# Optimization experiments

Measured on AMD Instinct MI355X. Metric: run time of the kernel, lower is better.

Reference implementation:

```python
import jax, jax.numpy as jnp
import numpy as np

N_NODES = 100000


def gcn_conv(x, edge_index, W, b, n_nodes):
    # PyG GCNConv: h = x @ W; add self-loops; symmetric normalization; aggregate to dst; + bias
    h = x @ W  # [N, out]
    loop = jnp.arange(n_nodes, dtype=edge_index.dtype)
    src = jnp.concatenate([edge_index[0], loop])
    dst = jnp.concatenate([edge_index[1], loop])
    ones = jnp.ones(src.shape[0], dtype=h.dtype)
    deg = jax.ops.segment_sum(ones, dst, num_segments=n_nodes)  # in-degree incl. self-loop
    dinv = jnp.where(deg > 0, jax.lax.rsqrt(deg), 0.0)
    norm = dinv[src] * dinv[dst]  # [E+N]
    msgs = h[src] * norm[:, None]  # gather + scale
    out = jax.ops.segment_sum(msgs, dst, num_segments=n_nodes)  # scatter-add
    return out + b


def setup_inputs() -> dict:
    key = jax.random.key(0)
    k1, k2, k3, k4 = jax.random.split(key, 4)
    x = jax.random.normal(k1, (N_NODES, 256), dtype=jnp.float32)
    edge_index = jax.random.randint(k2, (2, 3200000), 0, N_NODES, dtype=jnp.int64)
    W1 = jax.random.normal(k3, (256, 64), dtype=jnp.float32) * (1.0 / np.sqrt(256))
    b1 = jnp.zeros((64,), dtype=jnp.float32)
    W2 = jax.random.normal(k4, (64, 40), dtype=jnp.float32) * (1.0 / np.sqrt(64))
    b2 = jnp.zeros((40,), dtype=jnp.float32)
    return {"x": x, "edge_index": edge_index, "W1": W1, "b1": b1, "W2": W2, "b2": b2}


def reference(x, edge_index, W1, b1, W2, b2):
    n = x.shape[0]
    h = gcn_conv(x, edge_index, W1, b1, n)
    h = jax.nn.relu(h)
    h = gcn_conv(h, edge_index, W2, b2, n)
    return jax.nn.log_softmax(h, axis=1)
```

## Files before the change

kernel.cpp:

```cpp
#include <hip/hip_runtime.h>
#include <hip/hip_bf16.h>
#include <math.h>

static constexpr int NN    = 100000;
static constexpr int BSH   = 9;
static constexpr int NBUCK = (NN + 511) >> 9;
static constexpr int EPB   = 8192;
static constexpr int CAP   = 24576;

typedef __attribute__((ext_vector_type(8))) short short8;
typedef __attribute__((ext_vector_type(4))) float f32x4;
typedef __attribute__((ext_vector_type(2))) float f32x2;

#if defined(__has_builtin)
#  if __has_builtin(__builtin_amdgcn_cvt_pk_f32_fp8) && __has_builtin(__builtin_amdgcn_cvt_pk_fp8_f32)
#    define USE_HW_FP8 1
#  endif
#endif
#ifndef USE_HW_FP8
#  define USE_HW_FP8 0
#endif

__device__ __forceinline__ short f2bf(float f) {
    __hip_bfloat16 h = __float2bfloat16(f);
    return __builtin_bit_cast(short, h);
}

__device__ __forceinline__ float fp8_dec_sw(unsigned b) {
    unsigned u = ((b & 0x80u) << 24) | ((b & 0x7Fu) << 20);
    return __builtin_bit_cast(float, u) * 0x1p120f;
}
__device__ __forceinline__ unsigned fp8_enc_sw(float f) {
    unsigned u = __builtin_bit_cast(unsigned, f * 0x1p-120f);
    unsigned s = (u >> 24) & 0x80u;
    unsigned mag = u & 0x7FFFFFFFu;
    unsigned t = mag + 0x7FFFFu + ((mag >> 20) & 1u);
    unsigned r = t >> 20;
    if (r > 0x7Eu) r = 0x7Eu;
    return s | r;
}

template<bool HI>
__device__ __forceinline__ f32x2 dec2w(unsigned u) {
#if USE_HW_FP8
    return __builtin_amdgcn_cvt_pk_f32_fp8(u, HI);
#else
    unsigned w = HI ? (u >> 16) : u;
    f32x2 r;
    r.x = fp8_dec_sw(w & 0xFFu);
    r.y = fp8_dec_sw((w >> 8) & 0xFFu);
    return r;
#endif
}
__device__ __forceinline__ unsigned enc2(float a, float b) {
#if USE_HW_FP8
    return (unsigned)__builtin_amdgcn_cvt_pk_fp8_f32(a, b, 0, false);
#else
    return fp8_enc_sw(a) | (fp8_enc_sw(b) << 8);
#endif
}

__device__ __forceinline__ void acc8(f32x2* a, uint2 u) {
    a[0] += dec2w<false>(u.x);
    a[1] += dec2w<true>(u.x);
    a[2] += dec2w<false>(u.y);
    a[3] += dec2w<true>(u.y);
}
__device__ __forceinline__ void acc8s(f32x2* a, uint2 u, float ds) {
    f32x2 w = {ds, ds};
    a[0] = dec2w<false>(u.x) * w + a[0];
    a[1] = dec2w<true>(u.x)  * w + a[1];
    a[2] = dec2w<false>(u.y) * w + a[2];
    a[3] = dec2w<true>(u.y)  * w + a[3];
}

__device__ __forceinline__ long long ldidx(const void* __restrict__ p, long long i, int is64) {
    if (is64) return ((const long long* __restrict__)p)[i];
    return (long long)((const int* __restrict__)p)[i];
}

template<int K, int NCOLS, int KT, int NT>
__device__ __forceinline__ void packB_dev(const float* __restrict__ W,
                                          short* __restrict__ P, int t) {
    if (t >= KT * NT * 64) return;
    int kt = t / (NT * 64);
    int nt = (t / 64) % NT;
    int l  = t & 63;
    int g  = l >> 4;
#pragma unroll
    for (int e = 0; e < 8; ++e) {
        int k   = kt * 32 + g * 8 + e;
        int col = nt * 16 + (l & 15);
        float v = (col < NCOLS) ? W[k * NCOLS + col] : 0.0f;
        P[t * 8 + e] = f2bf(v);
    }
}

__global__ void __launch_bounds__(256)
k_init(const unsigned int* __restrict__ e32, int* __restrict__ flag,
       int* __restrict__ gcur,
       const float* __restrict__ W1, short* __restrict__ pB1,
       const float* __restrict__ W2, short* __restrict__ pB2) {
    int blk = blockIdx.x, tid = threadIdx.x;
    if (blk == 0) {
        if (tid < NBUCK) gcur[tid] = 0;
        __shared__ int any_nz;
        if (tid == 0) any_nz = 0;
        __syncthreads();
        unsigned int nz = 0;
        for (int w = 1 + 2 * tid; w < 4096; w += 512)
            nz |= e32[w];
        if (nz) atomicOr(&any_nz, 1);
        __syncthreads();
        if (tid == 0) *flag = (any_nz == 0) ? 1 : 0;
    } else if (blk <= 8) {
        packB_dev<256, 64, 8, 4>(W1, pB1, (blk - 1) * 256 + tid);
    } else {
        packB_dev<64, 40, 2, 3>(W2, pB2, (blk - 9) * 256 + tid);
    }
}

__global__ void __launch_bounds__(1024)
k_build_gemm1(const void* __restrict__ eidx, const int* __restrict__ flag, long long E,
              int nsblk, int ngblk, int* __restrict__ gcur, unsigned* __restrict__ ebuf,
              const float* __restrict__ X, const short* __restrict__ pB1,
              unsigned char* __restrict__ H, int n) {
    int bid = (int)blockIdx.x;
    int mn = nsblk < ngblk ? nsblk : ngblk;
    int role, idx;
    if (bid < 2 * mn) { role = bid & 1; idx = bid >> 1; }
    else {
        int rem = bid - 2 * mn;
        role = (nsblk > ngblk) ? 0 : 1;
        idx = mn + rem;
    }
    if (role == 0) {
        __shared__ int h[NBUCK];
        for (int b = threadIdx.x; b < NBUCK; b += 1024) h[b] = 0;
        __syncthreads();
        int is64 = *flag;
        long long base = (long long)idx * EPB;
        long long end  = base + EPB < E ? base + EPB : E;
        unsigned sv[8], dv[8];
        bool ok[8];
#pragma unroll
        for (int k = 0; k < 8; ++k) {
            long long e = base + (long long)k * 1024 + threadIdx.x;
            ok[k] = (e < end);
            if (ok[k]) {
                sv[k] = (unsigned)ldidx(eidx, e, is64);
                dv[k] = (unsigned)ldidx(eidx, E + e, is64);
                atomicAdd(&h[dv[k] >> BSH], 1);
            }
        }
        __syncthreads();
        for (int b = threadIdx.x; b < NBUCK; b += 1024)
            h[b] = atomicAdd(&gcur[b], h[b]);
        __syncthreads();
#pragma unroll
        for (int k = 0; k < 8; ++k) {
            if (ok[k]) {
                int bk = dv[k] >> BSH;
                int pos = atomicAdd(&h[bk], 1);
                ebuf[(long long)bk * CAP + pos] = sv[k] | ((dv[k] & 511u) << 17);
            }
        }
    } else {
        __shared__ alignas(16) short sW[8 * 4 * 512];
        __shared__ alignas(16) short sX[64 * 264];
        short8* dst = (short8*)sW;
        const short8* src = (const short8*)pB1;
        int tid = threadIdx.x;
        for (int i = tid; i < 2048; i += 1024) dst[i] = src[i];

        int wave = tid >> 6, lane = tid & 63;
        int g = lane >> 4;
        int wig = wave & 3;
        int grp = wave >> 2;

        int lr = tid >> 4;
        int c0 = (tid & 15) * 16;

        for (int s = 0; s < 4; ++s) {
            int grow = idx * 256 + s * 64 + lr;
            short* xd = &sX[lr * 264 + c0];
            if (grow < n) {
                const float* xr = X + (long long)grow * 256 + c0;
                float4 u0 = *(const float4*)(xr);
                float4 u1 = *(const float4*)(xr + 4);
                float4 u2 = *(const float4*)(xr + 8);
                float4 u3 = *(const float4*)(xr + 12);
                xd[0]  = f2bf(u0.x); xd[1]  = f2bf(u0.y); xd[2]  = f2bf(u0.z); xd[3]  = f2bf(u0.w);
                xd[4]  = f2bf(u1.x); xd[5]  = f2bf(u1.y); xd[6]  = f2bf(u1.z); xd[7]  = f2bf(u1.w);
                xd[8]  = f2bf(u2.x); xd[9]  = f2bf(u2.y); xd[10] = f2bf(u2.z); xd[11] = f2bf(u2.w);
                xd[12] = f2bf(u3.x); xd[13] = f2bf(u3.y); xd[14] = f2bf(u3.z); xd[15] = f2bf(u3.w);
            } else {
#pragma unroll
                for (int i = 0; i < 16; ++i) xd[i] = 0;
            }
            __syncthreads();
            if (grp == s) {
                f32x4 acc[4];
#pragma unroll
                for (int nt = 0; nt < 4; ++nt) acc[nt] = (f32x4){0.f, 0.f, 0.f, 0.f};
                const short* arow_p = &sX[(wig * 16 + (lane & 15)) * 264];
#pragma unroll
                for (int kt = 0; kt < 8; ++kt) {
                    short8 a = *(const short8*)(arow_p + kt * 32 + g * 8);
#pragma unroll
                    for (int nt = 0; nt < 4; ++nt) {
                        short8 bfr = dst[(kt * 4 + nt) * 64 + lane];
                        acc[nt] = __builtin_amdgcn_mfma_f32_16x16x32_bf16(a, bfr, acc[nt], 0, 0, 0);
                    }
                }
                int c = lane & 15;
                int orow_base = idx * 256 + s * 64 + wig * 16 + g * 4;
#pragma unroll
                for (int r = 0; r < 4; ++r) {
                    int orow = orow_base + r;
                    if (orow < n) {
                        unsigned char* hp = H + (long long)orow * 64;
#pragma unroll
                        for (int p = 0; p < 4; p += 2) {
                            unsigned wrd = enc2(acc[p][r], acc[p + 1][r]);
                            hp[p * 16 + c]       = (unsigned char)(wrd & 0xFFu);
                            hp[(p + 1) * 16 + c] = (unsigned char)((wrd >> 8) & 0xFFu);
                        }
                    }
                }
            }
            __syncthreads();
        }
    }
}

__global__ void __launch_bounds__(1024)
k_bucket_csr(const unsigned* __restrict__ ebuf, const int* __restrict__ gcnt,
             int* __restrict__ rowst, float* __restrict__ dinv,
             int* __restrict__ csr, int n) {
    __shared__ int cnt[512];
    __shared__ int cursor[512];
    __shared__ int woff[8];
    __shared__ int bs_sh;
    int b = blockIdx.x;
    int t = threadIdx.x;
    int cb = gcnt[b];
    long long rbase = (long long)b * CAP;
    if (t == 0) bs_sh = 0;
    if (t < 512) cnt[t] = 0;
    __syncthreads();
    if (t < b) atomicAdd(&bs_sh, gcnt[t]);
    for (int i = t; i < cb; i += 1024) {
        unsigned ed = ebuf[rbase + i];
        atomicAdd(&cnt[ed >> 17], 1);
    }
    __syncthreads();
    int bs = bs_sh;
    if (b == NBUCK - 1 && t == 0) rowst[n] = bs + cb;
    int v = 0, ps = 0;
    if (t < 512) {
        v = cnt[t];
        ps = v;
        int lane = t & 63;
#pragma unroll
        for (int off = 1; off < 64; off <<= 1) {
            int up = __shfl_up(ps, off);
            if (lane >= off) ps += up;
        }
        if (lane == 63) woff[t >> 6] = ps;
    }
    __syncthreads();
    if (t == 0) {
        int run = 0;
#pragma unroll
        for (int i = 0; i < 8; ++i) { int x = woff[i]; woff[i] = run; run += x; }
    }
    __syncthreads();
    if (t < 512) {
        int incl  = ps + woff[t >> 6];
        int start = bs + incl - v;
        int gnode = (b << BSH) + t;
        if (gnode < n) {
            rowst[gnode] = start;
            dinv[gnode]  = rsqrtf((float)(v + 1));
        }
        cursor[t] = start;
    }
    __syncthreads();
    for (int i = t; i < cb; i += 1024) {
        unsigned ed = ebuf[rbase + i];
        int pos = atomicAdd(&cursor[ed >> 17], 1);
        csr[pos] = (int)(ed & 0x1FFFFu);
    }
}

template<int K, int NCOLS, int KT, int NT, bool ABF16>
__global__ void __launch_bounds__(256)
k_mfma_gemm(const void* __restrict__ Xv, const short* __restrict__ packedB,
            const float* __restrict__ dinv, unsigned char* __restrict__ H, int n) {
    __shared__ alignas(16) short sW[KT * NT * 512];
    short8* dst = (short8*)sW;
    const short8* src = (const short8*)packedB;
    constexpr int TOT8 = KT * NT * 64;
    for (int i = threadIdx.x; i < TOT8; i += 256) dst[i] = src[i];
    __syncthreads();

    int wave = threadIdx.x >> 6, lane = threadIdx.x & 63;
    int g = lane >> 4;
    int arow = blockIdx.x * 64 + wave * 16 + (lane & 15);

    f32x4 acc[NT];
#pragma unroll
    for (int nt = 0; nt < NT; ++nt) acc[nt] = (f32x4){0.f, 0.f, 0.f, 0.f};

#pragma unroll
    for (int kt = 0; kt < KT; ++kt) {
        short8 a;
        if (arow < n) {
            int k0 = kt * 32 + g * 8;
            if (ABF16) {
                const short* xr = (const short*)Xv + (long long)arow * K;
                a = *(const short8*)(xr + k0);
            } else {
                const float* xr = (const float*)Xv + (long long)arow * K;
                float4 u = *(const float4*)(xr + k0);
                float4 v = *(const float4*)(xr + k0 + 4);
                a[0] = f2bf(u.x); a[1] = f2bf(u.y); a[2] = f2bf(u.z); a[3] = f2bf(u.w);
                a[4] = f2bf(v.x); a[5] = f2bf(v.y); a[6] = f2bf(v.z); a[7] = f2bf(v.w);
            }
        } else {
            a = (short8){0, 0, 0, 0, 0, 0, 0, 0};
        }
#pragma unroll
        for (int nt = 0; nt < NT; ++nt) {
            short8 bfr = dst[(kt * NT + nt) * 64 + lane];
            acc[nt] = __builtin_amdgcn_mfma_f32_16x16x32_bf16(a, bfr, acc[nt], 0, 0, 0);
        }
    }

    int c = lane & 15;
    int orow_base = blockIdx.x * 64 + wave * 16 + g * 4;
#pragma unroll
    for (int r = 0; r < 4; ++r) {
        int orow = orow_base + r;
        if (orow < n) {
            float di = dinv[orow];
            float v[NT];
#pragma unroll
            for (int nt = 0; nt < NT; ++nt) v[nt] = acc[nt][r] * di;
            unsigned char* hp = H + (long long)orow * NCOLS;
#pragma unroll
            for (int p = 0; p < NT; p += 2) {
                unsigned wrd = enc2(v[p], (p + 1 < NT) ? v[p + 1] : 0.0f);
                int col0 = p * 16 + c;
                if (col0 < NCOLS) hp[col0] = (unsigned char)(wrd & 0xFFu);
                if (p + 1 < NT) {
                    int col1 = col0 + 16;
                    if (col1 < NCOLS) hp[col1] = (unsigned char)((wrd >> 8) & 0xFFu);
                }
            }
        }
    }
}

__global__ void __launch_bounds__(256)
k_gather_relu(const int* __restrict__ rowst, const int* __restrict__ csr,
              const unsigned char* __restrict__ h1s, const float* __restrict__ dinv,
              const float* __restrict__ b, unsigned short* __restrict__ out, int n) {
    long long gid = (long long)blockIdx.x * blockDim.x + threadIdx.x;
    int node = (int)(gid >> 3);
    int fe   = (int)(gid & 7);
    if (node >= n) return;
    int jb = rowst[node], je = rowst[node + 1];
    unsigned feoff = (unsigned)fe << 3;

    f32x2 a0[4], a1[4], a2[4], a3[4];
#pragma unroll
    for (int q = 0; q < 4; ++q) {
        a0[q] = (f32x2){0.f, 0.f}; a1[q] = (f32x2){0.f, 0.f};
        a2[q] = (f32x2){0.f, 0.f}; a3[q] = (f32x2){0.f, 0.f};
    }

    int j = jb;
    for (; j + 3 < je; j += 4) {
        int s0 = csr[j], s1 = csr[j + 1], s2 = csr[j + 2], s3 = csr[j + 3];
        float ds0 = dinv[s0], ds1 = dinv[s1], ds2 = dinv[s2], ds3 = dinv[s3];
        uint2 u0 = *(const uint2*)(h1s + (((unsigned)s0 << 6) + feoff));
        uint2 u1 = *(const uint2*)(h1s + (((unsigned)s1 << 6) + feoff));
        uint2 u2 = *(const uint2*)(h1s + (((unsigned)s2 << 6) + feoff));
        uint2 u3 = *(const uint2*)(h1s + (((unsigned)s3 << 6) + feoff));
        acc8s(a0, u0, ds0);
        acc8s(a1, u1, ds1);
        acc8s(a2, u2, ds2);
        acc8s(a3, u3, ds3);
    }
    for (; j < je; ++j) {
        int s0 = csr[j];
        float ds0 = dinv[s0];
        uint2 u0 = *(const uint2*)(h1s + (((unsigned)s0 << 6) + feoff));
        acc8s(a0, u0, ds0);
    }
#pragma unroll
    for (int q = 0; q < 4; ++q) a0[q] += (a1[q] + a2[q]) + a3[q];

    float dn = dinv[node];
    uint2 self = *(const uint2*)(h1s + (((unsigned)node << 6) + feoff));
    acc8s(a0, self, dn);
    unsigned short r[8];
#pragma unroll
    for (int q = 0; q < 4; ++q) {
        float v0 = fmaxf(a0[q].x * dn + b[8 * fe + 2 * q],     0.0f);
        float v1 = fmaxf(a0[q].y * dn + b[8 * fe + 2 * q + 1], 0.0f);
        r[2 * q]     = (unsigned short)f2bf(v0);
        r[2 * q + 1] = (unsigned short)f2bf(v1);
    }
    uint4 pk;
    pk.x = (unsigned)r[0] | ((unsigned)r[1] << 16);
    pk.y = (unsigned)r[2] | ((unsigned)r[3] << 16);
    pk.z = (unsigned)r[4] | ((unsigned)r[5] << 16);
    pk.w = (unsigned)r[6] | ((unsigned)r[7] << 16);
    ((uint4*)(out + (long long)node * 64))[fe] = pk;
}

__global__ void __launch_bounds__(256)
k_gather_lsm(const int* __restrict__ rowst, const int* __restrict__ csr,
             const unsigned char* __restrict__ h2s, const float* __restrict__ dinv,
             const float* __restrict__ b, float* __restrict__ out, int n) {
    long long gid = (long long)blockIdx.x * blockDim.x + threadIdx.x;
    int node = (int)(gid >> 3);
    int fe   = (int)(gid & 7);
    if (node >= n) return;
    bool act = (fe < 5);
    int jb = rowst[node], je = rowst[node + 1];
    unsigned feoff = (unsigned)fe << 3;

    f32x2 a0[4], a1[4], a2[4], a3[4];
#pragma unroll
    for (int q = 0; q < 4; ++q) {
        a0[q] = (f32x2){0.f, 0.f}; a1[q] = (f32x2){0.f, 0.f};
        a2[q] = (f32x2){0.f, 0.f}; a3[q] = (f32x2){0.f, 0.f};
    }

    int j = jb;
    for (; j + 3 < je; j += 4) {
        int s0 = csr[j], s1 = csr[j + 1], s2 = csr[j + 2], s3 = csr[j + 3];
        if (act) {
            uint2 u0 = *(const uint2*)(h2s + ((unsigned)s0 * 40u + feoff));
            uint2 u1 = *(const uint2*)(h2s + ((unsigned)s1 * 40u + feoff));
            uint2 u2 = *(const uint2*)(h2s + ((unsigned)s2 * 40u + feoff));
            uint2 u3 = *(const uint2*)(h2s + ((unsigned)s3 * 40u + feoff));
            acc8(a0, u0);
            acc8(a1, u1);
            acc8(a2, u2);
            acc8(a3, u3);
        }
    }
    for (; j < je; ++j) {
        int s0 = csr[j];
        if (act) {
            uint2 u0 = *(const uint2*)(h2s + ((unsigned)s0 * 40u + feoff));
            acc8(a0, u0);
        }
    }
#pragma unroll
    for (int q = 0; q < 4; ++q) a0[q] += (a1[q] + a2[q]) + a3[q];

    float va[8];
    float mloc = -INFINITY;
    if (act) {
        uint2 self = *(const uint2*)(h2s + ((unsigned)node * 40u + feoff));
        acc8(a0, self);
        float di = dinv[node];
#pragma unroll
        for (int q = 0; q < 4; ++q) {
            va[2 * q]     = a0[q].x * di + b[8 * fe + 2 * q];
            va[2 * q + 1] = a0[q].y * di + b[8 * fe + 2 * q + 1];
            mloc = fmaxf(mloc, fmaxf(va[2 * q], va[2 * q + 1]));
        }
    }
    float m = mloc;
    m = fmaxf(m, __shfl_xor(m, 1));
    m = fmaxf(m, __shfl_xor(m, 2));
    m = fmaxf(m, __shfl_xor(m, 4));
    float ex = 0.0f;
    if (act) {
#pragma unroll
        for (int k = 0; k < 8; ++k) ex += __expf(va[k] - m);
    }
    ex += __shfl_xor(ex, 1);
    ex += __shfl_xor(ex, 2);
    ex += __shfl_xor(ex, 4);
    float lse = __logf(ex);
    if (act) {
        float4 r0 = make_float4(va[0] - m - lse, va[1] - m - lse,
                                va[2] - m - lse, va[3] - m - lse);
        float4 r1 = make_float4(va[4] - m - lse, va[5] - m - lse,
                                va[6] - m - lse, va[7] - m - lse);
        *(float4*)(out + (long long)node * 40 + 8 * fe)     = r0;
        *(float4*)(out + (long long)node * 40 + 8 * fe + 4) = r1;
    }
}

extern "C" void kernel_launch(void* const* d_in, const int* in_sizes, int n_in,
                              void* d_out, int out_size, void* d_ws, size_t ws_size,
                              hipStream_t stream) {
    const float* x  = (const float*)d_in[0];
    const void*  ei = d_in[1];
    const float* W1 = (const float*)d_in[2];
    const float* b1 = (const float*)d_in[3];
    const float* W2 = (const float*)d_in[4];
    const float* b2 = (const float*)d_in[5];
    float* out = (float*)d_out;

    const long long E = (long long)in_sizes[1] / 2;
    const int nsblk = (int)((E + EPB - 1) / EPB);
    const int ngblk = (NN + 255) / 256;

    char* w = (char*)d_ws;
    auto alloc = [&](size_t bytes) -> void* {
        void* p = (void*)w;
        w += (bytes + 255) & ~(size_t)255;
        return p;
    };
    int*      flag    = (int*)     alloc(4);
    int*      gcur    = (int*)     alloc((size_t)NBUCK * 4);
    int*      rowst   = (int*)     alloc(((size_t)NN + 1) * 4);
    float*    dinv    = (float*)   alloc((size_t)NN * 4);
    short*    pB1     = (short*)   alloc((size_t)8 * 4 * 64 * 8 * 2);
    short*    pB2     = (short*)   alloc((size_t)2 * 3 * 64 * 8 * 2);
    int*      csr     = (int*)     alloc((size_t)E * 4);
    unsigned* ebuf    = (unsigned*)alloc((size_t)NBUCK * CAP * 4);
    unsigned char* h1s = (unsigned char*)alloc((size_t)NN * 64);
    unsigned short* agg1 = (unsigned short*)alloc((size_t)NN * 64 * 2);
    unsigned char* h2s = h1s;

    const int B = 256;
    auto cdiv = [](long long a, long long b) { return (int)((a + b - 1) / b); };

    k_init<<<11, B, 0, stream>>>((const unsigned int*)ei, flag, gcur, W1, pB1, W2, pB2);

    k_build_gemm1<<<nsblk + ngblk, 1024, 0, stream>>>(ei, flag, E, nsblk, ngblk,
                                                      gcur, ebuf, x, pB1, h1s, NN);

    k_bucket_csr<<<NBUCK, 1024, 0, stream>>>(ebuf, gcur, rowst, dinv, csr, NN);

    k_gather_relu<<<cdiv((long long)NN * 8, B), B, 0, stream>>>(rowst, csr, h1s, dinv, b1, agg1, NN);

    k_mfma_gemm<64, 40, 2, 3, true><<<cdiv(NN, 64), B, 0, stream>>>(agg1, pB2, dinv, h2s, NN);

    k_gather_lsm<<<cdiv((long long)NN * 8, B), B, 0, stream>>>(rowst, csr, h2s, dinv, b2, out, NN);
}
```

Baseline: 179.6 us.

## Split fused scatter/GEMM1 kernel into separate scatter and 256-thread GEMM kernels

Replaces the single heterogeneous kernel, which interleaved edge-bucket scatter blocks with GEMM1 blocks, with two separate launches. GEMM1 now uses 256-thread blocks covering 64 rows each, with all waves doing MFMA work, instead of 1024-thread blocks where only a quarter of the waves computed per stage. The X tile is written to shared memory with vectorized short8 stores. The scatter and GEMM phases no longer overlap within one launch, and there is one more kernel launch.

```diff
diff --git a/kernel.cpp b/kernel.cpp
--- a/kernel.cpp
+++ b/kernel.cpp
@@ -6,6 +6,7 @@
 static constexpr int BSH   = 9;
 static constexpr int NBUCK = (NN + 511) >> 9;
 static constexpr int EPB   = 8192;
+static constexpr int SCT   = 1024;
 static constexpr int CAP   = 24576;
 
 typedef __attribute__((ext_vector_type(8))) short short8;
@@ -120,116 +121,105 @@
     }
 }
 
-__global__ void __launch_bounds__(1024)
-k_build_gemm1(const void* __restrict__ eidx, const int* __restrict__ flag, long long E,
-              int nsblk, int ngblk, int* __restrict__ gcur, unsigned* __restrict__ ebuf,
-              const float* __restrict__ X, const short* __restrict__ pB1,
-              unsigned char* __restrict__ H, int n) {
-    int bid = (int)blockIdx.x;
-    int mn = nsblk < ngblk ? nsblk : ngblk;
-    int role, idx;
-    if (bid < 2 * mn) { role = bid & 1; idx = bid >> 1; }
-    else {
-        int rem = bid - 2 * mn;
-        role = (nsblk > ngblk) ? 0 : 1;
-        idx = mn + rem;
-    }
-    if (role == 0) {
-        __shared__ int h[NBUCK];
-        for (int b = threadIdx.x; b < NBUCK; b += 1024) h[b] = 0;
-        __syncthreads();
-        int is64 = *flag;
-        long long base = (long long)idx * EPB;
-        long long end  = base + EPB < E ? base + EPB : E;
-        unsigned sv[8], dv[8];
-        bool ok[8];
-#pragma unroll
-        for (int k = 0; k < 8; ++k) {
-            long long e = base + (long long)k * 1024 + threadIdx.x;
-            ok[k] = (e < end);
-            if (ok[k]) {
-                sv[k] = (unsigned)ldidx(eidx, e, is64);
-                dv[k] = (unsigned)ldidx(eidx, E + e, is64);
-                atomicAdd(&h[dv[k] >> BSH], 1);
+__global__ void __launch_bounds__(SCT)
+k_scatter_bucket(const void* __restrict__ eidx, const int* __restrict__ flag, long long E,
+                 int* __restrict__ gcur, unsigned* __restrict__ ebuf) {
+    __shared__ int h[NBUCK];
+    for (int b = threadIdx.x; b < NBUCK; b += SCT) h[b] = 0;
+    __syncthreads();
+    int is64 = *flag;
+    long long base = (long long)blockIdx.x * EPB;
+    long long end  = base + EPB < E ? base + EPB : E;
+    unsigned sv[8], dv[8];
+    bool ok[8];
+#pragma unroll
+    for (int k = 0; k < 8; ++k) {
+        long long e = base + (long long)k * SCT + threadIdx.x;
+        ok[k] = (e < end);
+        if (ok[k]) {
+            sv[k] = (unsigned)ldidx(eidx, e, is64);
+            dv[k] = (unsigned)ldidx(eidx, E + e, is64);
+            atomicAdd(&h[dv[k] >> BSH], 1);
+        }
+    }
+    __syncthreads();
+    for (int b = threadIdx.x; b < NBUCK; b += SCT)
+        h[b] = atomicAdd(&gcur[b], h[b]);
+    __syncthreads();
+#pragma unroll
+    for (int k = 0; k < 8; ++k) {
+        if (ok[k]) {
+            int bk = dv[k] >> BSH;
+            int pos = atomicAdd(&h[bk], 1);
+            ebuf[(long long)bk * CAP + pos] = sv[k] | ((dv[k] & 511u) << 17);
+        }
+    }
+}
+
+__global__ void __launch_bounds__(256)
+k_gemm1(const float* __restrict__ X, const short* __restrict__ pB1,
+        unsigned char* __restrict__ H, int n) {
+    __shared__ alignas(16) short sW[8 * 4 * 512];
+    __shared__ alignas(16) short sX[64 * 264];
+    short8* dst = (short8*)sW;
+    const short8* src = (const short8*)pB1;
+    int tid = threadIdx.x;
+    for (int i = tid; i < 2048; i += 256) dst[i] = src[i];
+
+    int rb = blockIdx.x * 64;
+    int c0 = (tid & 15) * 16;
+#pragma unroll
+    for (int p = 0; p < 4; ++p) {
+        int lr = p * 16 + (tid >> 4);
+        int grow = rb + lr;
+        short8 lo, hi;
+        if (grow < n) {
+            const float* xr = X + (long long)grow * 256 + c0;
+            float4 u0 = *(const float4*)(xr);
+            float4 u1 = *(const float4*)(xr + 4);
+            float4 u2 = *(const float4*)(xr + 8);
+            float4 u3 = *(const float4*)(xr + 12);
+            lo[0] = f2bf(u0.x); lo[1] = f2bf(u0.y); lo[2] = f2bf(u0.z); lo[3] = f2bf(u0.w);
+            lo[4] = f2bf(u1.x); lo[5] = f2bf(u1.y); lo[6] = f2bf(u1.z); lo[7] = f2bf(u1.w);
+            hi[0] = f2bf(u2.x); hi[1] = f2bf(u2.y); hi[2] = f2bf(u2.z); hi[3] = f2bf(u2.w);
+            hi[4] = f2bf(u3.x); hi[5] = f2bf(u3.y); hi[6] = f2bf(u3.z); hi[7] = f2bf(u3.w);
+        } else {
+            lo = (short8){0,0,0,0,0,0,0,0};
+            hi = lo;
+        }
+        *(short8*)&sX[lr * 264 + c0]     = lo;
+        *(short8*)&sX[lr * 264 + c0 + 8] = hi;
+    }
+    __syncthreads();
+
+    int wave = tid >> 6, lane = tid & 63;
+    int g = lane >> 4;
+    f32x4 acc[4];
+#pragma unroll
+    for (int nt = 0; nt < 4; ++nt) acc[nt] = (f32x4){0.f, 0.f, 0.f, 0.f};
+    const short* arow_p = &sX[(wave * 16 + (lane & 15)) * 264];
+#pragma unroll
+    for (int kt = 0; kt < 8; ++kt) {
+        short8 a = *(const short8*)(arow_p + kt * 32 + g * 8);
+#pragma unroll
+        for (int nt = 0; nt < 4; ++nt) {
+            short8 bfr = dst[(kt * 4 + nt) * 64 + lane];
+            acc[nt] = __builtin_amdgcn_mfma_f32_16x16x32_bf16(a, bfr, acc[nt], 0, 0, 0);
+        }
+    }
+    int c = lane & 15;
+    int orow_base = rb + wave * 16 + g * 4;
+#pragma unroll
+    for (int r = 0; r < 4; ++r) {
+        int orow = orow_base + r;
+        if (orow < n) {
+            unsigned char* hp = H + (long long)orow * 64;
+#pragma unroll
+            for (int p = 0; p < 4; p += 2) {
+                unsigned wrd = enc2(acc[p][r], acc[p + 1][r]);
+                hp[p * 16 + c]       = (unsigned char)(wrd & 0xFFu);
+                hp[(p + 1) * 16 + c] = (unsigned char)((wrd >> 8) & 0xFFu);
             }
-        }
-        __syncthreads();
-        for (int b = threadIdx.x; b < NBUCK; b += 1024)
-            h[b] = atomicAdd(&gcur[b], h[b]);
-        __syncthreads();
-#pragma unroll
-        for (int k = 0; k < 8; ++k) {
-            if (ok[k]) {
-                int bk = dv[k] >> BSH;
-                int pos = atomicAdd(&h[bk], 1);
-                ebuf[(long long)bk * CAP + pos] = sv[k] | ((dv[k] & 511u) << 17);
-            }
-        }
-    } else {
-        __shared__ alignas(16) short sW[8 * 4 * 512];
-        __shared__ alignas(16) short sX[64 * 264];
-        short8* dst = (short8*)sW;
-        const short8* src = (const short8*)pB1;
-        int tid = threadIdx.x;
-        for (int i = tid; i < 2048; i += 1024) dst[i] = src[i];
-
-        int wave = tid >> 6, lane = tid & 63;
-        int g = lane >> 4;
-        int wig = wave & 3;
-        int grp = wave >> 2;
-
-        int lr = tid >> 4;
-        int c0 = (tid & 15) * 16;
-
-        for (int s = 0; s < 4; ++s) {
-            int grow = idx * 256 + s * 64 + lr;
-            short* xd = &sX[lr * 264 + c0];
-            if (grow < n) {
-                const float* xr = X + (long long)grow * 256 + c0;
-                float4 u0 = *(const float4*)(xr);
-                float4 u1 = *(const float4*)(xr + 4);
-                float4 u2 = *(const float4*)(xr + 8);
-                float4 u3 = *(const float4*)(xr + 12);
-                xd[0]  = f2bf(u0.x); xd[1]  = f2bf(u0.y); xd[2]  = f2bf(u0.z); xd[3]  = f2bf(u0.w);
-                xd[4]  = f2bf(u1.x); xd[5]  = f2bf(u1.y); xd[6]  = f2bf(u1.z); xd[7]  = f2bf(u1.w);
-                xd[8]  = f2bf(u2.x); xd[9]  = f2bf(u2.y); xd[10] = f2bf(u2.z); xd[11] = f2bf(u2.w);
-                xd[12] = f2bf(u3.x); xd[13] = f2bf(u3.y); xd[14] = f2bf(u3.z); xd[15] = f2bf(u3.w);
-            } else {
-#pragma unroll
-                for (int i = 0; i < 16; ++i) xd[i] = 0;
-            }
-            __syncthreads();
-            if (grp == s) {
-                f32x4 acc[4];
-#pragma unroll
-                for (int nt = 0; nt < 4; ++nt) acc[nt] = (f32x4){0.f, 0.f, 0.f, 0.f};
-                const short* arow_p = &sX[(wig * 16 + (lane & 15)) * 264];
-#pragma unroll
-                for (int kt = 0; kt < 8; ++kt) {
-                    short8 a = *(const short8*)(arow_p + kt * 32 + g * 8);
-#pragma unroll
-                    for (int nt = 0; nt < 4; ++nt) {
-                        short8 bfr = dst[(kt * 4 + nt) * 64 + lane];
-                        acc[nt] = __builtin_amdgcn_mfma_f32_16x16x32_bf16(a, bfr, acc[nt], 0, 0, 0);
-                    }
-                }
-                int c = lane & 15;
-                int orow_base = idx * 256 + s * 64 + wig * 16 + g * 4;
-#pragma unroll
-                for (int r = 0; r < 4; ++r) {
-                    int orow = orow_base + r;
-                    if (orow < n) {
-                        unsigned char* hp = H + (long long)orow * 64;
-#pragma unroll
-                        for (int p = 0; p < 4; p += 2) {
-                            unsigned wrd = enc2(acc[p][r], acc[p + 1][r]);
-                            hp[p * 16 + c]       = (unsigned char)(wrd & 0xFFu);
-                            hp[(p + 1) * 16 + c] = (unsigned char)((wrd >> 8) & 0xFFu);
-                        }
-                    }
-                }
-            }
-            __syncthreads();
         }
     }
 }
@@ -514,7 +504,7 @@
 
     const long long E = (long long)in_sizes[1] / 2;
     const int nsblk = (int)((E + EPB - 1) / EPB);
-    const int ngblk = (NN + 255) / 256;
+    const int ngblk = (NN + 63) / 64;
 
     char* w = (char*)d_ws;
     auto alloc = [&](size_t bytes) -> void* {
@@ -539,8 +529,9 @@
 
     k_init<<<11, B, 0, stream>>>((const unsigned int*)ei, flag, gcur, W1, pB1, W2, pB2);
 
-    k_build_gemm1<<<nsblk + ngblk, 1024, 0, stream>>>(ei, flag, E, nsblk, ngblk,
-                                                      gcur, ebuf, x, pB1, h1s, NN);
+    k_scatter_bucket<<<nsblk, SCT, 0, stream>>>(ei, flag, E, gcur, ebuf);
+
+    k_gemm1<<<ngblk, B, 0, stream>>>(x, pB1, h1s, NN);
 
     k_bucket_csr<<<NBUCK, 1024, 0, stream>>>(ebuf, gcur, rowst, dinv, csr, NN);
 
```

Result: slower. 189.0 us (+5.2%).

## Spread GEMM tile work across all 16 waves and vectorize LDS staging

Applied to the files above, without the earlier changes.

The X@W1 tile stage previously had only 4 of 16 waves doing MFMA per 64-row sub-tile (grp==s), each computing 4 column tiles. Now every wave computes one 16x16 output tile (wig selects rows, nt selects column tile), so all waves work on each sub-tile. The fp32->bf16 converted row is also written to LDS as two short8 vector stores, after the first barrier, instead of 16 scalar short stores. Each FP8 output byte is now encoded individually, with no pair packing, which adds some redundant conversion work.

```diff
diff --git a/kernel.cpp b/kernel.cpp
--- a/kernel.cpp
+++ b/kernel.cpp
@@ -174,62 +174,52 @@
         for (int i = tid; i < 2048; i += 1024) dst[i] = src[i];
 
         int wave = tid >> 6, lane = tid & 63;
-        int g = lane >> 4;
-        int wig = wave & 3;
-        int grp = wave >> 2;
+        int g   = lane >> 4;
+        int wig = wave >> 2;
+        int nt  = wave & 3;
 
         int lr = tid >> 4;
         int c0 = (tid & 15) * 16;
 
         for (int s = 0; s < 4; ++s) {
             int grow = idx * 256 + s * 64 + lr;
-            short* xd = &sX[lr * 264 + c0];
+            short8 lo, hi;
             if (grow < n) {
                 const float* xr = X + (long long)grow * 256 + c0;
                 float4 u0 = *(const float4*)(xr);
                 float4 u1 = *(const float4*)(xr + 4);
                 float4 u2 = *(const float4*)(xr + 8);
                 float4 u3 = *(const float4*)(xr + 12);
-                xd[0]  = f2bf(u0.x); xd[1]  = f2bf(u0.y); xd[2]  = f2bf(u0.z); xd[3]  = f2bf(u0.w);
-                xd[4]  = f2bf(u1.x); xd[5]  = f2bf(u1.y); xd[6]  = f2bf(u1.z); xd[7]  = f2bf(u1.w);
-                xd[8]  = f2bf(u2.x); xd[9]  = f2bf(u2.y); xd[10] = f2bf(u2.z); xd[11] = f2bf(u2.w);
-                xd[12] = f2bf(u3.x); xd[13] = f2bf(u3.y); xd[14] = f2bf(u3.z); xd[15] = f2bf(u3.w);
+                lo[0] = f2bf(u0.x); lo[1] = f2bf(u0.y); lo[2] = f2bf(u0.z); lo[3] = f2bf(u0.w);
+                lo[4] = f2bf(u1.x); lo[5] = f2bf(u1.y); lo[6] = f2bf(u1.z); lo[7] = f2bf(u1.w);
+                hi[0] = f2bf(u2.x); hi[1] = f2bf(u2.y); hi[2] = f2bf(u2.z); hi[3] = f2bf(u2.w);
+                hi[4] = f2bf(u3.x); hi[5] = f2bf(u3.y); hi[6] = f2bf(u3.z); hi[7] = f2bf(u3.w);
             } else {
-#pragma unroll
-                for (int i = 0; i < 16; ++i) xd[i] = 0;
+                lo = (short8){0,0,0,0,0,0,0,0};
+                hi = lo;
             }
             __syncthreads();
-            if (grp == s) {
-                f32x4 acc[4];
-#pragma unroll
-                for (int nt = 0; nt < 4; ++nt) acc[nt] = (f32x4){0.f, 0.f, 0.f, 0.f};
-                const short* arow_p = &sX[(wig * 16 + (lane & 15)) * 264];
-#pragma unroll
-                for (int kt = 0; kt < 8; ++kt) {
-                    short8 a = *(const short8*)(arow_p + kt * 32 + g * 8);
-#pragma unroll
-                    for (int nt = 0; nt < 4; ++nt) {
-                        short8 bfr = dst[(kt * 4 + nt) * 64 + lane];
-                        acc[nt] = __builtin_amdgcn_mfma_f32_16x16x32_bf16(a, bfr, acc[nt], 0, 0, 0);
-                    }
-                }
-                int c = lane & 15;
-                int orow_base = idx * 256 + s * 64 + wig * 16 + g * 4;
-#pragma unroll
-                for (int r = 0; r < 4; ++r) {
-                    int orow = orow_base + r;
-                    if (orow < n) {
-                        unsigned char* hp = H + (long long)orow * 64;
-#pragma unroll
-                        for (int p = 0; p < 4; p += 2) {
-                            unsigned wrd = enc2(acc[p][r], acc[p + 1][r]);
-                            hp[p * 16 + c]       = (unsigned char)(wrd & 0xFFu);
-                            hp[(p + 1) * 16 + c] = (unsigned char)((wrd >> 8) & 0xFFu);
-                        }
-                    }
-                }
-            }
+            *(short8*)&sX[lr * 264 + c0]     = lo;
+            *(short8*)&sX[lr * 264 + c0 + 8] = hi;
             __syncthreads();
+
+            f32x4 acc = (f32x4){0.f, 0.f, 0.f, 0.f};
+            const short* arow_p = &sX[(wig * 16 + (lane & 15)) * 264];
+#pragma unroll
+            for (int kt = 0; kt < 8; ++kt) {
+                short8 a = *(const short8*)(arow_p + kt * 32 + g * 8);
+                short8 bfr = dst[(kt * 4 + nt) * 64 + lane];
+                acc = __builtin_amdgcn_mfma_f32_16x16x32_bf16(a, bfr, acc, 0, 0, 0);
+            }
+            int c = nt * 16 + (lane & 15);
+            int orow_base = idx * 256 + s * 64 + wig * 16 + g * 4;
+#pragma unroll
+            for (int r = 0; r < 4; ++r) {
+                int orow = orow_base + r;
+                if (orow < n)
+                    H[(long long)orow * 64 + c] =
+                        (unsigned char)(enc2(acc[r], 0.0f) & 0xFFu);
+            }
         }
     }
 }
```

Measured after the change: 179.2 us. About the same (-0.2%).
